# Optimization experiments

Hardware: AMD Instinct MI355X
Metric: run time of the kernel (lower is better)

Reference implementation:

```python
import jax, jax.numpy as jnp
import numpy as np

B, C, D, H, W = 2, 3, 4, 32, 32
N = D * H * W
REAL_SIZE = jnp.array([3.0, 25.0, 25.0], dtype=jnp.float32)
CUTOFFS = jnp.array([1.0, 0.75], dtype=jnp.float32)   # cutoff[c-1] for class c in {1,2}
SPLIT = [0.0, 3.0 + 1e-5]                             # split[-1] += 1e-5 as in __init__
S = len(SPLIT) - 1
NMS_ITERS = 32  # fixed-point iterations; greedy-NMS update is idempotent once converged


def setup_inputs() -> dict:
    key = jax.random.key(0)
    k1, k2, k3, k4 = jax.random.split(key, 4)
    return {
        "pred_clses": jax.random.normal(k1, (B, C, D, H, W), dtype=jnp.float32),
        "pred_boxes": jax.random.normal(k2, (B, 3, D, H, W), dtype=jnp.float32),
        "targ_clses": jax.random.randint(k3, (B, D, H, W), 0, C),
        "targ_boxes": jax.random.uniform(k4, (B, D, H, W, 3), dtype=jnp.float32),
    }


def _pdist2(a, b):
    # squared euclidean cdist without materializing [N,N,3]
    aa = (a * a).sum(-1)
    bb = (b * b).sum(-1)
    return jnp.maximum(aa[:, None] + bb[None, :] - 2.0 * (a @ b.T), 0.0)


def _grid():
    d, h, w = jnp.meshgrid(jnp.arange(D), jnp.arange(H), jnp.arange(W), indexing="ij")
    return jnp.stack([d, h, w], -1).reshape(N, 3).astype(jnp.float32)


def _confusion(pred_pos, conf, pred_arg, targ_pos, targ_cls, c, cutoff):
    # mask-based (fixed-shape, jit-safe) version of the per-(batch,class) loop body
    valid_p = pred_arg == c
    # self.sort: confidence-descending order (invalid points pushed to the end)
    order = jnp.argsort(-jnp.where(valid_p, conf, -jnp.inf))
    pos = pred_pos[order]      # [N,3] physical coords (already * real_size)
    valid = valid_p[order]
    c2 = cutoff * cutoff
    # triu conflict graph restricted to valid points; order fixed => shrinking
    # DIS[SELECT][:,SELECT] in the original == masking rows/cols by 'alive' here
    conflict = (_pdist2(pos, pos) < c2) & jnp.triu(jnp.ones((N, N), bool), 1) \
               & valid[:, None] & valid[None, :]

    def body(_, alive):
        Mf = (conflict & alive[:, None] & alive[None, :]).astype(jnp.float32)
        restrain = Mf.sum(0)
        restrain = restrain - (restrain != 0).astype(jnp.float32) @ Mf
        return alive & (restrain == 0)

    alive = jax.lax.fori_loop(0, NMS_ITERS, body, valid)  # NMS fixed point

    # match(): targets hit by any surviving prediction within cutoff
    valid_t = targ_cls == c
    matched = ((_pdist2(pos, targ_pos) < c2) & alive[:, None]).any(0)
    z_p, z_t = pos[:, 0], targ_pos[:, 0]
    rows = []
    for i in range(S):
        lo, hi = SPLIT[i], SPLIT[i + 1]
        lp = alive & (z_p >= lo) & (z_p < hi)
        lt = valid_t & (z_t >= lo) & (z_t < hi)
        tp = (lt & matched).sum()
        rows.append(jnp.stack([tp, lp.sum() - tp, lt.sum() - tp]))  # TP, FP, FN
    return jnp.stack(rows)  # [S,3]


def _forward(pred_clses, pred_boxes, targ_clses, targ_boxes):
    grid, dims = _grid(), jnp.array([D, H, W], jnp.float32)
    pc = pred_clses.transpose(0, 2, 3, 4, 1).reshape(B, N, C)
    conf, arg = pc.max(-1), pc.argmax(-1)
    pb = jax.nn.sigmoid(pred_boxes.transpose(0, 2, 3, 4, 1).reshape(B, N, 3))
    # boxncls2pos: (voxel index + in-cell offset) / grid dims -> [0,1]^3, then * real_size
    pred_pos = (grid + pb) / dims * REAL_SIZE
    targ_pos = (grid + targ_boxes.reshape(B, N, 3)) / dims * REAL_SIZE
    tcls = targ_clses.reshape(B, N)
    cs = jnp.arange(1, C)
    per_cls = jax.vmap(_confusion, in_axes=(None, None, None, None, None, 0, 0))
    per_b = jax.vmap(per_cls, in_axes=(0, 0, 0, 0, 0, None, None))
    return per_b(pred_pos, conf, arg, targ_pos, tcls, cs, CUTOFFS)  # [B, C-1, S, 3]


def reference(pred_clses, pred_boxes, targ_clses, targ_boxes):
    return _forward(pred_clses, pred_boxes, targ_clses, targ_boxes)
```

## Files before the change

### kernel.cpp

```cpp
#include <hip/hip_runtime.h>
#include <cstdint>
#include <cstddef>

typedef unsigned long long u64;
typedef unsigned int u32;
typedef unsigned short u16;

#define N_ 4096
#define MMAX_ 2048
#define KCAP_ 32
#define SENT_ 2048

__device__ __forceinline__ float sigf(float x) { return 1.0f / (1.0f + expf(-x)); }

#define ANY4(arr, wa, wb) \
  ((int)((arr)[(wa) & 0xFFFFu] | (arr)[(wa) >> 16] | \
         (arr)[(wb) & 0xFFFFu] | (arr)[(wb) >> 16]))
#define GRPSCAN(arr, dw, dg, outAny) do { \
  outAny = ANY4(arr, dw[0], dw[1]); \
  if ((dg) > 4) { outAny |= ANY4(arr, dw[2], dw[3]); \
  if ((dg) > 8) { outAny |= ANY4(arr, dw[4], dw[5]); \
  if ((dg) > 12) { outAny |= ANY4(arr, dw[6], dw[7]); \
  if ((dg) > 16) { outAny |= ANY4(arr, dw[8], dw[9]); \
  if ((dg) > 20) { outAny |= ANY4(arr, dw[10], dw[11]); \
  if ((dg) > 24) { outAny |= ANY4(arr, dw[12], dw[13]); \
  if ((dg) > 28) { outAny |= ANY4(arr, dw[14], dw[15]); }}}}}}} \
} while (0)

__global__ __launch_bounds__(1024) void k_compact(
    const float* __restrict__ pc, const float* __restrict__ pb,
    int* __restrict__ Mcnt, float4* __restrict__ posG, u16* __restrict__ slotG,
    float4* __restrict__ sp4, float4* __restrict__ alivePosG) {
  int pair = blockIdx.x, b = pair >> 1, c = (pair & 1) + 1;
  int tid = threadIdx.x, lane = tid & 63;
  __shared__ int cnt;
  if (tid == 0) cnt = 0;
  __syncthreads();
  const float* pcb = pc + (size_t)b * 3 * N_;
  const float* pbb = pb + (size_t)b * 3 * N_;
  for (int base = 0; base < N_; base += 1024) {
    int n = base + tid;
    float v0 = pcb[n], v1 = pcb[n + N_], v2 = pcb[n + 2 * N_];
    float cf = v0; int a = 0;
    if (v1 > cf) { cf = v1; a = 1; }
    if (v2 > cf) { cf = v2; a = 2; }
    bool valid = (a == c);
    u32 o = __float_as_uint(cf);
    o ^= (o >> 31) ? 0xFFFFFFFFu : 0x80000000u;
    u64 ball = __ballot(valid);
    int wbase = 0;
    if (lane == 0 && ball) wbase = atomicAdd(&cnt, __popcll(ball));
    wbase = __shfl(wbase, 0);
    int p = wbase + __popcll(ball & ((1ull << lane) - 1ull));
    float4 dead; dead.x = 1e9f; dead.y = 1e9f; dead.z = 1e9f; dead.w = 0.f;
    alivePosG[pair * N_ + n] = dead;
    if (valid && p < MMAX_) {
      float d = (float)(n >> 10), h = (float)((n >> 5) & 31), w = (float)(n & 31);
      float x = (d + sigf(pbb[n])) * 0.75f;
      float y = (h + sigf(pbb[n + N_])) * 0.78125f;
      float z = (w + sigf(pbb[n + 2 * N_])) * 0.78125f;
      float4 vg; vg.x = x; vg.y = y; vg.z = z; vg.w = __uint_as_float(o);
      posG[pair * N_ + n] = vg;
      slotG[pair * N_ + n] = (u16)p;
      float4 vs; vs.x = x; vs.y = y; vs.z = z; vs.w = __uint_as_float((u32)n);
      sp4[pair * MMAX_ + p] = vs;
    } else {
      posG[pair * N_ + n] = dead;
      slotG[pair * N_ + n] = (u16)0xFFFF;
    }
  }
  __syncthreads();
  if (tid == 0) {
    int M = cnt; if (M > MMAX_) M = MMAX_;
    Mcnt[pair] = M;
  }
}

template <int EXT>
__device__ __forceinline__ void adj_body(
    const float4* __restrict__ posG, const u16* __restrict__ slotG,
    int* __restrict__ deg, u16* __restrict__ predL, int pair, int n, int slot,
    float cut2) {
  float4 self = posG[pair * N_ + n];
  u32 okey = __float_as_uint(self.w);
  int d0 = n >> 10, h0 = (n >> 5) & 31, w0 = n & 31;
  u16* rowp = predL + (((size_t)pair * MMAX_ + slot) << 5);
  int cnt = 0;
  #pragma unroll
  for (int dd = -EXT; dd <= EXT; ++dd) {
    #pragma unroll
    for (int dh = -EXT; dh <= EXT; ++dh) {
      #pragma unroll
      for (int dw = -EXT; dw <= EXT; ++dw) {
        if (dd == 0 && dh == 0 && dw == 0) continue;
        if ((dd * dd == 4) + (dh * dh == 4) + (dw * dw == 4) > 1) continue;
        int d2i = d0 + dd, h2i = h0 + dh, w2i = w0 + dw;
        if ((u32)d2i < 4u && (u32)h2i < 32u && (u32)w2i < 32u) {
          int n2 = (d2i << 10) | (h2i << 5) | w2i;
          float4 pn = posG[pair * N_ + n2];
          float dx = pn.x - self.x, dy = pn.y - self.y, dz = pn.z - self.z;
          float dsq = dx * dx + dy * dy + dz * dz;
          u32 ok2 = __float_as_uint(pn.w);
          bool pred = (dsq < cut2) && (ok2 > okey || (ok2 == okey && n2 < n));
          if (pred) {
            u16 s2 = slotG[pair * N_ + n2];
            if (cnt < KCAP_) rowp[cnt] = s2;
            cnt++;
          }
        }
      }
    }
  }
  if (cnt > KCAP_) cnt = KCAP_;
  deg[pair * MMAX_ + slot] = cnt;
  int pad = (cnt + 3) & ~3;
  for (int s = cnt; s < pad; ++s) rowp[s] = (u16)SENT_;
}

__global__ __launch_bounds__(256) void k_adj(
    const float4* __restrict__ posG, const u16* __restrict__ slotG,
    int* __restrict__ deg, u16* __restrict__ predL) {
  int idx = blockIdx.x * 256 + threadIdx.x;
  int pair = idx >> 12, n = idx & (N_ - 1);
  int slot = slotG[pair * N_ + n];
  if (slot == 0xFFFF) return;
  if (pair & 1) adj_body<1>(posG, slotG, deg, predL, pair, n, slot, 0.5625f);
  else          adj_body<2>(posG, slotG, deg, predL, pair, n, slot, 1.0f);
}

__global__ __launch_bounds__(1024) void k_nms(
    const int* __restrict__ Mcnt, const int* __restrict__ deg,
    const u16* __restrict__ predL, const float4* __restrict__ sp4,
    float4* __restrict__ alivePosG, int* __restrict__ out) {
  int pair = blockIdx.x;
  int tid = threadIdx.x;
  int M = Mcnt[pair];
  __shared__ unsigned char aliveB[2064];
  __shared__ unsigned char freeB[2064];
  __shared__ int flag[2], acnt;
  int r0 = tid, r1 = tid + 1024;
  int dg0 = deg[pair * MMAX_ + r0];
  int dg1 = deg[pair * MMAX_ + r1];
  u32 dw0[16], dw1[16];
  {
    const uint4* p0 = (const uint4*)(predL + (((size_t)pair * MMAX_ + r0) << 5));
    const uint4* p1 = (const uint4*)(predL + (((size_t)pair * MMAX_ + r1) << 5));
    #pragma unroll
    for (int q = 0; q < 4; ++q) {
      uint4 t0 = p0[q];
      dw0[4 * q] = t0.x; dw0[4 * q + 1] = t0.y; dw0[4 * q + 2] = t0.z; dw0[4 * q + 3] = t0.w;
      uint4 t1 = p1[q];
      dw1[4 * q] = t1.x; dw1[4 * q + 1] = t1.y; dw1[4 * q + 2] = t1.z; dw1[4 * q + 3] = t1.w;
    }
  }
  bool a0 = (r0 < M), a1 = (r1 < M);
  aliveB[r0] = a0; aliveB[r1] = a1;
  freeB[r0] = 0; freeB[r1] = 0;
  if (tid < 16) { aliveB[2048 + tid] = 0; freeB[2048 + tid] = 0; }
  if (tid == 0) { flag[0] = 0; flag[1] = 0; acnt = 0; }
  __syncthreads();

  for (int iter = 0; iter < 32; ++iter) {
    if (tid == 0) flag[(iter + 1) & 1] = 0;
    bool fr0 = a0, fr1 = a1;
    if (a0 && dg0) { int any; GRPSCAN(aliveB, dw0, dg0, any); fr0 = (any == 0); }
    if (a1 && dg1) { int any; GRPSCAN(aliveB, dw1, dg1, any); fr1 = (any == 0); }
    freeB[r0] = fr0; freeB[r1] = fr1;
    __syncthreads();
    int lch = 0;
    if (a0 && dg0) { int any; GRPSCAN(freeB, dw0, dg0, any); if (any) { a0 = false; aliveB[r0] = 0; lch = 1; } }
    if (a1 && dg1) { int any; GRPSCAN(freeB, dw1, dg1, any); if (any) { a1 = false; aliveB[r1] = 0; lch = 1; } }
    if (lch) flag[iter & 1] = 1;
    __syncthreads();
    if (!flag[iter & 1]) break;
  }

  if (a0) {
    float4 v = sp4[pair * MMAX_ + r0];
    alivePosG[pair * N_ + (int)__float_as_uint(v.w)] = v;
  }
  if (a1) {
    float4 v = sp4[pair * MMAX_ + r1];
    alivePosG[pair * N_ + (int)__float_as_uint(v.w)] = v;
  }
  {
    u64 ball = __ballot(a0);
    if ((tid & 63) == 0 && ball) atomicAdd(&acnt, __popcll(ball));
  }
  {
    u64 ball = __ballot(a1);
    if ((tid & 63) == 0 && ball) atomicAdd(&acnt, __popcll(ball));
  }
  __syncthreads();
  if (tid == 0) {
    int A = acnt;
    out[pair * 3 + 0] = 0;
    out[pair * 3 + 1] = A;
    out[pair * 3 + 2] = 0;
  }
}

template <int EXT>
__device__ __forceinline__ int match_ball(
    const float4* __restrict__ alive, int n, float tx, float ty, float tz,
    float cut2) {
  int d0 = n >> 10, h0 = (n >> 5) & 31, w0 = n & 31;
  int m = 0;
  #pragma unroll
  for (int dd = -EXT; dd <= EXT; ++dd) {
    #pragma unroll
    for (int dh = -EXT; dh <= EXT; ++dh) {
      #pragma unroll
      for (int dw = -EXT; dw <= EXT; ++dw) {
        if ((dd * dd == 4) + (dh * dh == 4) + (dw * dw == 4) > 1) continue;
        int d2i = d0 + dd, h2i = h0 + dh, w2i = w0 + dw;
        if ((u32)d2i < 4u && (u32)h2i < 32u && (u32)w2i < 32u) {
          int n2 = (d2i << 10) | (h2i << 5) | w2i;
          float4 p = alive[n2];
          float dx = p.x - tx, dy = p.y - ty, dz = p.z - tz;
          m |= (int)(dx * dx + dy * dy + dz * dz < cut2);
        }
      }
    }
  }
  return m;
}

__global__ __launch_bounds__(256) void k_match(
    const float4* __restrict__ alivePosG,
    const int* __restrict__ tcls, const float* __restrict__ tb,
    int* __restrict__ out) {
  int idx = blockIdx.x * 256 + threadIdx.x;
  int pair = idx >> 12, n = idx & (N_ - 1);
  int b = pair >> 1, c = (pair & 1) + 1;
  float cut2 = (pair & 1) ? 0.5625f : 1.0f;
  __shared__ int s_tp, s_t;
  if (threadIdx.x == 0) { s_tp = 0; s_t = 0; }
  __syncthreads();
  int isC = (tcls[b * N_ + n] == c) ? 1 : 0;
  float d = (float)(n >> 10), h = (float)((n >> 5) & 31), w = (float)(n & 31);
  const float* tbp = tb + ((size_t)b * N_ + n) * 3;
  float tx = (d + tbp[0]) * 0.75f;
  float ty = (h + tbp[1]) * 0.78125f;
  float tz = (w + tbp[2]) * 0.78125f;
  const float4* alive = alivePosG + (size_t)pair * N_;
  int m;
  if (pair & 1) m = match_ball<1>(alive, n, tx, ty, tz, cut2);
  else          m = match_ball<2>(alive, n, tx, ty, tz, cut2);
  m &= isC;
  atomicAdd(&s_tp, m);
  atomicAdd(&s_t, isC);
  __syncthreads();
  if (threadIdx.x == 0) {
    atomicAdd(&out[pair * 3 + 0], s_tp);
    atomicAdd(&out[pair * 3 + 1], -s_tp);
    atomicAdd(&out[pair * 3 + 2], s_t - s_tp);
  }
}

extern "C" void kernel_launch(void* const* d_in, const int* in_sizes, int n_in,
                              void* d_out, int out_size, void* d_ws, size_t ws_size,
                              hipStream_t stream) {
  (void)in_sizes; (void)n_in; (void)out_size; (void)ws_size;
  const float* pc = (const float*)d_in[0];
  const float* pb = (const float*)d_in[1];
  const int*   tc = (const int*)d_in[2];
  const float* tb = (const float*)d_in[3];
  int* out = (int*)d_out;

  char* ws = (char*)d_ws;
  size_t off = 0;
  auto alloc = [&](size_t bytes) -> void* {
    void* p = ws + off;
    off += (bytes + 255) & ~(size_t)255;
    return p;
  };
  int*    Mcnt      = (int*)alloc(4 * 4);
  float4* posG      = (float4*)alloc((size_t)4 * N_ * 16);
  u16*    slotG     = (u16*)alloc((size_t)4 * N_ * 2);
  float4* sp4       = (float4*)alloc((size_t)4 * MMAX_ * 16);
  int*    deg       = (int*)alloc((size_t)4 * MMAX_ * 4);
  u16*    predL     = (u16*)alloc((size_t)4 * MMAX_ * KCAP_ * 2);
  float4* alivePosG = (float4*)alloc((size_t)4 * N_ * 16);

  k_compact<<<4, 1024, 0, stream>>>(pc, pb, Mcnt, posG, slotG, sp4, alivePosG);
  k_adj<<<(4 * N_) / 256, 256, 0, stream>>>(posG, slotG, deg, predL);
  k_nms<<<4, 1024, 0, stream>>>(Mcnt, deg, predL, sp4, alivePosG, out);
  k_match<<<(4 * N_) / 256, 256, 0, stream>>>(alivePosG, tc, tb, out);
}
```

Before: 106.4 us.

## Fuse four kernels into one cooperative kernel with grid syncs

```diff
diff --git a/kernel.cpp b/kernel.cpp
--- a/kernel.cpp
+++ b/kernel.cpp
@@ -1,6 +1,9 @@
 #include <hip/hip_runtime.h>
+#include <hip/hip_cooperative_groups.h>
 #include <cstdint>
 #include <cstddef>
+
+namespace cg = cooperative_groups;
 
 typedef unsigned long long u64;
 typedef unsigned int u32;
@@ -13,33 +16,91 @@
 
 __device__ __forceinline__ float sigf(float x) { return 1.0f / (1.0f + expf(-x)); }
 
-#define ANY4(arr, wa, wb) \
+template <int EXT>
+__device__ __forceinline__ void adj_body(
+    const float4* __restrict__ posG, const u16* __restrict__ slotG,
+    int* __restrict__ deg, u16* __restrict__ predL, int pair, int n, int slot,
+    float cut2) {
+  float4 self = posG[pair * N_ + n];
+  u32 okey = __float_as_uint(self.w);
+  int d0 = n >> 10, h0 = (n >> 5) & 31, w0 = n & 31;
+  u16* rowp = predL + (((size_t)pair * MMAX_ + slot) << 5);
+  int cnt = 0;
+  #pragma unroll
+  for (int dd = -EXT; dd <= EXT; ++dd) {
+    #pragma unroll
+    for (int dh = -EXT; dh <= EXT; ++dh) {
+      #pragma unroll
+      for (int dw = -EXT; dw <= EXT; ++dw) {
+        if (dd == 0 && dh == 0 && dw == 0) continue;
+        if ((dd * dd == 4) + (dh * dh == 4) + (dw * dw == 4) > 1) continue;
+        int d2i = d0 + dd, h2i = h0 + dh, w2i = w0 + dw;
+        if ((u32)d2i < 4u && (u32)h2i < 32u && (u32)w2i < 32u) {
+          int n2 = (d2i << 10) | (h2i << 5) | w2i;
+          float4 pn = posG[pair * N_ + n2];
+          float dx = pn.x - self.x, dy = pn.y - self.y, dz = pn.z - self.z;
+          float dsq = dx * dx + dy * dy + dz * dz;
+          u32 ok2 = __float_as_uint(pn.w);
+          bool pred = (dsq < cut2) && (ok2 > okey || (ok2 == okey && n2 < n));
+          if (pred) {
+            u16 s2 = slotG[pair * N_ + n2];
+            if (cnt < KCAP_) rowp[cnt] = s2;
+            cnt++;
+          }
+        }
+      }
+    }
+  }
+  if (cnt > KCAP_) cnt = KCAP_;
+  deg[pair * MMAX_ + slot] = cnt;
+  int pad = (cnt + 3) & ~3;
+  for (int s = cnt; s < pad; ++s) rowp[s] = (u16)SENT_;
+}
+
+template <int EXT>
+__device__ __forceinline__ int match_ball(
+    const float4* __restrict__ alive, int n, float tx, float ty, float tz,
+    float cut2) {
+  int d0 = n >> 10, h0 = (n >> 5) & 31, w0 = n & 31;
+  int m = 0;
+  #pragma unroll
+  for (int dd = -EXT; dd <= EXT; ++dd) {
+    #pragma unroll
+    for (int dh = -EXT; dh <= EXT; ++dh) {
+      #pragma unroll
+      for (int dw = -EXT; dw <= EXT; ++dw) {
+        if ((dd * dd == 4) + (dh * dh == 4) + (dw * dw == 4) > 1) continue;
+        int d2i = d0 + dd, h2i = h0 + dh, w2i = w0 + dw;
+        if ((u32)d2i < 4u && (u32)h2i < 32u && (u32)w2i < 32u) {
+          int n2 = (d2i << 10) | (h2i << 5) | w2i;
+          float4 p = alive[n2];
+          float dx = p.x - tx, dy = p.y - ty, dz = p.z - tz;
+          m |= (int)(dx * dx + dy * dy + dz * dz < cut2);
+        }
+      }
+    }
+  }
+  return m;
+}
+
+#define ANY4B(arr, wa, wb) \
   ((int)((arr)[(wa) & 0xFFFFu] | (arr)[(wa) >> 16] | \
          (arr)[(wb) & 0xFFFFu] | (arr)[(wb) >> 16]))
-#define GRPSCAN(arr, dw, dg, outAny) do { \
-  outAny = ANY4(arr, dw[0], dw[1]); \
-  if ((dg) > 4) { outAny |= ANY4(arr, dw[2], dw[3]); \
-  if ((dg) > 8) { outAny |= ANY4(arr, dw[4], dw[5]); \
-  if ((dg) > 12) { outAny |= ANY4(arr, dw[6], dw[7]); \
-  if ((dg) > 16) { outAny |= ANY4(arr, dw[8], dw[9]); \
-  if ((dg) > 20) { outAny |= ANY4(arr, dw[10], dw[11]); \
-  if ((dg) > 24) { outAny |= ANY4(arr, dw[12], dw[13]); \
-  if ((dg) > 28) { outAny |= ANY4(arr, dw[14], dw[15]); }}}}}}} \
-} while (0)
-
-__global__ __launch_bounds__(1024) void k_compact(
+
+__global__ __launch_bounds__(256) void k_all(
     const float* __restrict__ pc, const float* __restrict__ pb,
-    int* __restrict__ Mcnt, float4* __restrict__ posG, u16* __restrict__ slotG,
-    float4* __restrict__ sp4, float4* __restrict__ alivePosG) {
-  int pair = blockIdx.x, b = pair >> 1, c = (pair & 1) + 1;
-  int tid = threadIdx.x, lane = tid & 63;
-  __shared__ int cnt;
-  if (tid == 0) cnt = 0;
-  __syncthreads();
-  const float* pcb = pc + (size_t)b * 3 * N_;
-  const float* pbb = pb + (size_t)b * 3 * N_;
-  for (int base = 0; base < N_; base += 1024) {
-    int n = base + tid;
+    const int* __restrict__ tcls, const float* __restrict__ tb,
+    int* __restrict__ cntG, float4* __restrict__ posG, u16* __restrict__ slotG,
+    float4* __restrict__ sp4, int* __restrict__ deg, u16* __restrict__ predL,
+    float4* __restrict__ alivePosG, int* __restrict__ out) {
+  cg::grid_group grid = cg::this_grid();
+  int blk = blockIdx.x, tid = threadIdx.x, lane = tid & 63;
+
+  {
+    int pair = blk >> 4, b = pair >> 1, c = (pair & 1) + 1;
+    int n = ((blk & 15) << 8) | tid;
+    const float* pcb = pc + (size_t)b * 3 * N_;
+    const float* pbb = pb + (size_t)b * 3 * N_;
     float v0 = pcb[n], v1 = pcb[n + N_], v2 = pcb[n + 2 * N_];
     float cf = v0; int a = 0;
     if (v1 > cf) { cf = v1; a = 1; }
@@ -49,7 +110,7 @@
     o ^= (o >> 31) ? 0xFFFFFFFFu : 0x80000000u;
     u64 ball = __ballot(valid);
     int wbase = 0;
-    if (lane == 0 && ball) wbase = atomicAdd(&cnt, __popcll(ball));
+    if (lane == 0 && ball) wbase = atomicAdd(&cntG[pair], __popcll(ball));
     wbase = __shfl(wbase, 0);
     int p = wbase + __popcll(ball & ((1ull << lane) - 1ull));
     float4 dead; dead.x = 1e9f; dead.y = 1e9f; dead.z = 1e9f; dead.w = 0.f;
@@ -69,192 +130,121 @@
       slotG[pair * N_ + n] = (u16)0xFFFF;
     }
   }
-  __syncthreads();
-  if (tid == 0) {
-    int M = cnt; if (M > MMAX_) M = MMAX_;
-    Mcnt[pair] = M;
-  }
-}
-
-template <int EXT>
-__device__ __forceinline__ void adj_body(
-    const float4* __restrict__ posG, const u16* __restrict__ slotG,
-    int* __restrict__ deg, u16* __restrict__ predL, int pair, int n, int slot,
-    float cut2) {
-  float4 self = posG[pair * N_ + n];
-  u32 okey = __float_as_uint(self.w);
-  int d0 = n >> 10, h0 = (n >> 5) & 31, w0 = n & 31;
-  u16* rowp = predL + (((size_t)pair * MMAX_ + slot) << 5);
-  int cnt = 0;
-  #pragma unroll
-  for (int dd = -EXT; dd <= EXT; ++dd) {
-    #pragma unroll
-    for (int dh = -EXT; dh <= EXT; ++dh) {
-      #pragma unroll
-      for (int dw = -EXT; dw <= EXT; ++dw) {
-        if (dd == 0 && dh == 0 && dw == 0) continue;
-        if ((dd * dd == 4) + (dh * dh == 4) + (dw * dw == 4) > 1) continue;
-        int d2i = d0 + dd, h2i = h0 + dh, w2i = w0 + dw;
-        if ((u32)d2i < 4u && (u32)h2i < 32u && (u32)w2i < 32u) {
-          int n2 = (d2i << 10) | (h2i << 5) | w2i;
-          float4 pn = posG[pair * N_ + n2];
-          float dx = pn.x - self.x, dy = pn.y - self.y, dz = pn.z - self.z;
-          float dsq = dx * dx + dy * dy + dz * dz;
-          u32 ok2 = __float_as_uint(pn.w);
-          bool pred = (dsq < cut2) && (ok2 > okey || (ok2 == okey && n2 < n));
-          if (pred) {
-            u16 s2 = slotG[pair * N_ + n2];
-            if (cnt < KCAP_) rowp[cnt] = s2;
-            cnt++;
-          }
-        }
-      }
-    }
-  }
-  if (cnt > KCAP_) cnt = KCAP_;
-  deg[pair * MMAX_ + slot] = cnt;
-  int pad = (cnt + 3) & ~3;
-  for (int s = cnt; s < pad; ++s) rowp[s] = (u16)SENT_;
-}
-
-__global__ __launch_bounds__(256) void k_adj(
-    const float4* __restrict__ posG, const u16* __restrict__ slotG,
-    int* __restrict__ deg, u16* __restrict__ predL) {
-  int idx = blockIdx.x * 256 + threadIdx.x;
-  int pair = idx >> 12, n = idx & (N_ - 1);
-  int slot = slotG[pair * N_ + n];
-  if (slot == 0xFFFF) return;
-  if (pair & 1) adj_body<1>(posG, slotG, deg, predL, pair, n, slot, 0.5625f);
-  else          adj_body<2>(posG, slotG, deg, predL, pair, n, slot, 1.0f);
-}
-
-__global__ __launch_bounds__(1024) void k_nms(
-    const int* __restrict__ Mcnt, const int* __restrict__ deg,
-    const u16* __restrict__ predL, const float4* __restrict__ sp4,
-    float4* __restrict__ alivePosG, int* __restrict__ out) {
-  int pair = blockIdx.x;
-  int tid = threadIdx.x;
-  int M = Mcnt[pair];
+  grid.sync();
+
+  {
+    int idx = (blk << 8) | tid;
+    int pair = idx >> 12, n = idx & (N_ - 1);
+    int slot = slotG[pair * N_ + n];
+    if (slot != 0xFFFF) {
+      if (pair & 1) adj_body<1>(posG, slotG, deg, predL, pair, n, slot, 0.5625f);
+      else          adj_body<2>(posG, slotG, deg, predL, pair, n, slot, 1.0f);
+    }
+  }
+  grid.sync();
+
   __shared__ unsigned char aliveB[2064];
   __shared__ unsigned char freeB[2064];
   __shared__ int flag[2], acnt;
-  int r0 = tid, r1 = tid + 1024;
-  int dg0 = deg[pair * MMAX_ + r0];
-  int dg1 = deg[pair * MMAX_ + r1];
-  u32 dw0[16], dw1[16];
+  if (blk < 4) {
+    int pair = blk;
+    int M = cntG[pair]; if (M > MMAX_) M = MMAX_;
+    int dg[8]; u32 pw[8][4]; bool al[8];
+    #pragma unroll
+    for (int q = 0; q < 8; ++q) {
+      int r = tid + (q << 8);
+      al[q] = (r < M);
+      dg[q] = deg[pair * MMAX_ + r];
+      uint4 t = *(const uint4*)(predL + (((size_t)pair * MMAX_ + r) << 5));
+      pw[q][0] = t.x; pw[q][1] = t.y; pw[q][2] = t.z; pw[q][3] = t.w;
+      aliveB[r] = al[q];
+      freeB[r] = 0;
+    }
+    if (tid < 16) { aliveB[2048 + tid] = 0; freeB[2048 + tid] = 0; }
+    if (tid == 0) { flag[0] = 0; flag[1] = 0; acnt = 0; }
+    __syncthreads();
+    for (int iter = 0; iter < 32; ++iter) {
+      if (tid == 0) flag[(iter + 1) & 1] = 0;
+      #pragma unroll
+      for (int q = 0; q < 8; ++q) {
+        int r = tid + (q << 8);
+        bool fr = al[q];
+        if (al[q] && dg[q]) {
+          int any = ANY4B(aliveB, pw[q][0], pw[q][1]);
+          if (dg[q] > 4) any |= ANY4B(aliveB, pw[q][2], pw[q][3]);
+          if (dg[q] > 8) {
+            const u16* rowp = predL + (((size_t)pair * MMAX_ + r) << 5);
+            for (int k = 8; k < dg[q]; ++k) any |= aliveB[rowp[k]];
+          }
+          fr = (any == 0);
+        }
+        freeB[r] = fr;
+      }
+      __syncthreads();
+      int lch = 0;
+      #pragma unroll
+      for (int q = 0; q < 8; ++q) {
+        int r = tid + (q << 8);
+        if (al[q] && dg[q]) {
+          int any = ANY4B(freeB, pw[q][0], pw[q][1]);
+          if (dg[q] > 4) any |= ANY4B(freeB, pw[q][2], pw[q][3]);
+          if (dg[q] > 8) {
+            const u16* rowp = predL + (((size_t)pair * MMAX_ + r) << 5);
+            for (int k = 8; k < dg[q]; ++k) any |= freeB[rowp[k]];
+          }
+          if (any) { al[q] = false; aliveB[r] = 0; lch = 1; }
+        }
+      }
+      if (lch) flag[iter & 1] = 1;
+      __syncthreads();
+      if (!flag[iter & 1]) break;
+    }
+    int cntA = 0;
+    #pragma unroll
+    for (int q = 0; q < 8; ++q) {
+      if (al[q]) {
+        cntA++;
+        float4 v = sp4[pair * MMAX_ + tid + (q << 8)];
+        alivePosG[pair * N_ + (int)__float_as_uint(v.w)] = v;
+      }
+    }
+    if (cntA) atomicAdd(&acnt, cntA);
+    __syncthreads();
+    if (tid == 0) {
+      out[pair * 3 + 0] = 0;
+      out[pair * 3 + 1] = acnt;
+      out[pair * 3 + 2] = 0;
+    }
+  }
+  grid.sync();
+
   {
-    const uint4* p0 = (const uint4*)(predL + (((size_t)pair * MMAX_ + r0) << 5));
-    const uint4* p1 = (const uint4*)(predL + (((size_t)pair * MMAX_ + r1) << 5));
-    #pragma unroll
-    for (int q = 0; q < 4; ++q) {
-      uint4 t0 = p0[q];
-      dw0[4 * q] = t0.x; dw0[4 * q + 1] = t0.y; dw0[4 * q + 2] = t0.z; dw0[4 * q + 3] = t0.w;
-      uint4 t1 = p1[q];
-      dw1[4 * q] = t1.x; dw1[4 * q + 1] = t1.y; dw1[4 * q + 2] = t1.z; dw1[4 * q + 3] = t1.w;
-    }
-  }
-  bool a0 = (r0 < M), a1 = (r1 < M);
-  aliveB[r0] = a0; aliveB[r1] = a1;
-  freeB[r0] = 0; freeB[r1] = 0;
-  if (tid < 16) { aliveB[2048 + tid] = 0; freeB[2048 + tid] = 0; }
-  if (tid == 0) { flag[0] = 0; flag[1] = 0; acnt = 0; }
-  __syncthreads();
-
-  for (int iter = 0; iter < 32; ++iter) {
-    if (tid == 0) flag[(iter + 1) & 1] = 0;
-    bool fr0 = a0, fr1 = a1;
-    if (a0 && dg0) { int any; GRPSCAN(aliveB, dw0, dg0, any); fr0 = (any == 0); }
-    if (a1 && dg1) { int any; GRPSCAN(aliveB, dw1, dg1, any); fr1 = (any == 0); }
-    freeB[r0] = fr0; freeB[r1] = fr1;
-    __syncthreads();
-    int lch = 0;
-    if (a0 && dg0) { int any; GRPSCAN(freeB, dw0, dg0, any); if (any) { a0 = false; aliveB[r0] = 0; lch = 1; } }
-    if (a1 && dg1) { int any; GRPSCAN(freeB, dw1, dg1, any); if (any) { a1 = false; aliveB[r1] = 0; lch = 1; } }
-    if (lch) flag[iter & 1] = 1;
-    __syncthreads();
-    if (!flag[iter & 1]) break;
-  }
-
-  if (a0) {
-    float4 v = sp4[pair * MMAX_ + r0];
-    alivePosG[pair * N_ + (int)__float_as_uint(v.w)] = v;
-  }
-  if (a1) {
-    float4 v = sp4[pair * MMAX_ + r1];
-    alivePosG[pair * N_ + (int)__float_as_uint(v.w)] = v;
-  }
-  {
-    u64 ball = __ballot(a0);
-    if ((tid & 63) == 0 && ball) atomicAdd(&acnt, __popcll(ball));
-  }
-  {
-    u64 ball = __ballot(a1);
-    if ((tid & 63) == 0 && ball) atomicAdd(&acnt, __popcll(ball));
-  }
-  __syncthreads();
-  if (tid == 0) {
-    int A = acnt;
-    out[pair * 3 + 0] = 0;
-    out[pair * 3 + 1] = A;
-    out[pair * 3 + 2] = 0;
-  }
-}
-
-template <int EXT>
-__device__ __forceinline__ int match_ball(
-    const float4* __restrict__ alive, int n, float tx, float ty, float tz,
-    float cut2) {
-  int d0 = n >> 10, h0 = (n >> 5) & 31, w0 = n & 31;
-  int m = 0;
-  #pragma unroll
-  for (int dd = -EXT; dd <= EXT; ++dd) {
-    #pragma unroll
-    for (int dh = -EXT; dh <= EXT; ++dh) {
-      #pragma unroll
-      for (int dw = -EXT; dw <= EXT; ++dw) {
-        if ((dd * dd == 4) + (dh * dh == 4) + (dw * dw == 4) > 1) continue;
-        int d2i = d0 + dd, h2i = h0 + dh, w2i = w0 + dw;
-        if ((u32)d2i < 4u && (u32)h2i < 32u && (u32)w2i < 32u) {
-          int n2 = (d2i << 10) | (h2i << 5) | w2i;
-          float4 p = alive[n2];
-          float dx = p.x - tx, dy = p.y - ty, dz = p.z - tz;
-          m |= (int)(dx * dx + dy * dy + dz * dz < cut2);
-        }
-      }
-    }
-  }
-  return m;
-}
-
-__global__ __launch_bounds__(256) void k_match(
-    const float4* __restrict__ alivePosG,
-    const int* __restrict__ tcls, const float* __restrict__ tb,
-    int* __restrict__ out) {
-  int idx = blockIdx.x * 256 + threadIdx.x;
-  int pair = idx >> 12, n = idx & (N_ - 1);
-  int b = pair >> 1, c = (pair & 1) + 1;
-  float cut2 = (pair & 1) ? 0.5625f : 1.0f;
-  __shared__ int s_tp, s_t;
-  if (threadIdx.x == 0) { s_tp = 0; s_t = 0; }
-  __syncthreads();
-  int isC = (tcls[b * N_ + n] == c) ? 1 : 0;
-  float d = (float)(n >> 10), h = (float)((n >> 5) & 31), w = (float)(n & 31);
-  const float* tbp = tb + ((size_t)b * N_ + n) * 3;
-  float tx = (d + tbp[0]) * 0.75f;
-  float ty = (h + tbp[1]) * 0.78125f;
-  float tz = (w + tbp[2]) * 0.78125f;
-  const float4* alive = alivePosG + (size_t)pair * N_;
-  int m;
-  if (pair & 1) m = match_ball<1>(alive, n, tx, ty, tz, cut2);
-  else          m = match_ball<2>(alive, n, tx, ty, tz, cut2);
-  m &= isC;
-  atomicAdd(&s_tp, m);
-  atomicAdd(&s_t, isC);
-  __syncthreads();
-  if (threadIdx.x == 0) {
-    atomicAdd(&out[pair * 3 + 0], s_tp);
-    atomicAdd(&out[pair * 3 + 1], -s_tp);
-    atomicAdd(&out[pair * 3 + 2], s_t - s_tp);
+    int idx = (blk << 8) | tid;
+    int pair = idx >> 12, n = idx & (N_ - 1);
+    int b = pair >> 1, c = (pair & 1) + 1;
+    float cut2 = (pair & 1) ? 0.5625f : 1.0f;
+    __shared__ int s_tp, s_t;
+    if (tid == 0) { s_tp = 0; s_t = 0; }
+    __syncthreads();
+    int isC = (tcls[b * N_ + n] == c) ? 1 : 0;
+    float d = (float)(n >> 10), h = (float)((n >> 5) & 31), w = (float)(n & 31);
+    const float* tbp = tb + ((size_t)b * N_ + n) * 3;
+    float tx = (d + tbp[0]) * 0.75f;
+    float ty = (h + tbp[1]) * 0.78125f;
+    float tz = (w + tbp[2]) * 0.78125f;
+    const float4* alive = alivePosG + (size_t)pair * N_;
+    int m;
+    if (pair & 1) m = match_ball<1>(alive, n, tx, ty, tz, cut2);
+    else          m = match_ball<2>(alive, n, tx, ty, tz, cut2);
+    m &= isC;
+    atomicAdd(&s_tp, m);
+    atomicAdd(&s_t, isC);
+    __syncthreads();
+    if (tid == 0) {
+      atomicAdd(&out[pair * 3 + 0], s_tp);
+      atomicAdd(&out[pair * 3 + 1], -s_tp);
+      atomicAdd(&out[pair * 3 + 2], s_t - s_tp);
+    }
   }
 }
 
@@ -275,7 +265,7 @@
     off += (bytes + 255) & ~(size_t)255;
     return p;
   };
-  int*    Mcnt      = (int*)alloc(4 * 4);
+  int*    cntG      = (int*)alloc(4 * 4);
   float4* posG      = (float4*)alloc((size_t)4 * N_ * 16);
   u16*    slotG     = (u16*)alloc((size_t)4 * N_ * 2);
   float4* sp4       = (float4*)alloc((size_t)4 * MMAX_ * 16);
@@ -283,8 +273,13 @@
   u16*    predL     = (u16*)alloc((size_t)4 * MMAX_ * KCAP_ * 2);
   float4* alivePosG = (float4*)alloc((size_t)4 * N_ * 16);
 
-  k_compact<<<4, 1024, 0, stream>>>(pc, pb, Mcnt, posG, slotG, sp4, alivePosG);
-  k_adj<<<(4 * N_) / 256, 256, 0, stream>>>(posG, slotG, deg, predL);
-  k_nms<<<4, 1024, 0, stream>>>(Mcnt, deg, predL, sp4, alivePosG, out);
-  k_match<<<(4 * N_) / 256, 256, 0, stream>>>(alivePosG, tc, tb, out);
-}
+  hipMemsetAsync(cntG, 0, 4 * sizeof(int), stream);
+
+  void* args[] = {
+    (void*)&pc, (void*)&pb, (void*)&tc, (void*)&tb,
+    (void*)&cntG, (void*)&posG, (void*)&slotG, (void*)&sp4,
+    (void*)&deg, (void*)&predL, (void*)&alivePosG, (void*)&out
+  };
+  hipLaunchCooperativeKernel((const void*)k_all, dim3(64), dim3(256),
+                             args, 0, stream);
+}
```

After: 155.0 us. 45.7% more time.
